# Kernel optimization log

Hardware: AMD Instinct MI355X
Metric: run time of the kernel (lower is better)

## Reference

```python
import jax, jax.numpy as jnp
import numpy as np

EPS = 1e-5
T = 5          # Newton-Schulz iterations
G = 64         # num_groups
FACTOR = 1.0   # reparameterization scale


def setup_inputs() -> dict:
    key = jax.random.key(0)
    k1, k2, k3, k4 = jax.random.split(key, 4)
    B, C, H, W = 32, 256, 64, 64
    x = jax.random.normal(k1, (B, C, H, W), dtype=jnp.float32)
    idx = jax.random.permutation(k2, C)                      # random channel shuffle
    eps1 = jax.random.normal(k3, (B, G, G), dtype=jnp.float32)  # randn_like(wm_inv)
    eps2 = jax.random.normal(k4, (B, G, 1), dtype=jnp.float32)  # randn_like(mean)
    return {"x": x, "idx": idx, "eps1": eps1, "eps2": eps2}


def _sqrtvar(t):
    # torch .var(dim=0) is unbiased (ddof=1); repeat over batch == broadcast
    return jnp.sqrt(jnp.var(t, axis=0, keepdims=True, ddof=1) + EPS)


def reference(x, idx, eps1, eps2):
    B, C, H, W = x.shape
    # reverse permutation: reverse_idx[idx[i]] = i
    reverse_idx = jnp.zeros_like(idx).at[idx].set(jnp.arange(C, dtype=idx.dtype))

    xs = x[:, idx].reshape(B, G, -1)          # [B, G, m], m = (C//G)*H*W
    m = xs.shape[-1]
    mean = xs.mean(-1, keepdims=True)         # [B, G, 1]
    xm = xs - mean

    sigma = jnp.einsum('bgm,bhm->bgh', xm, xm) / m   # [B, G, G]
    I = jnp.eye(G, dtype=x.dtype)
    trace_inv = 1.0 / jnp.trace(sigma, axis1=1, axis2=2)[:, None, None]
    sigma_N = sigma * trace_inv

    # Newton-Schulz inverse square root: P <- 1.5 P - 0.5 P^3 sigma_N
    P = jnp.broadcast_to(I, sigma.shape)
    for _ in range(T):
        P = 1.5 * P - 0.5 * ((P @ P @ P) @ sigma_N)
    wm = P * jnp.sqrt(trace_inv)

    # faithful to original b_inv: solve(I, wm) == wm (original code quirk)
    wm_inv = jnp.linalg.solve(jnp.broadcast_to(I, wm.shape), wm)

    # stochastic reparameterization of gamma (symmetrized via triu) and beta
    wir = wm_inv + (eps1 * FACTOR) * _sqrtvar(wm_inv)
    gamma = jnp.triu(wir) + jnp.swapaxes(jnp.triu(wir, k=1), 1, 2)
    beta = mean + (eps2 * FACTOR) * _sqrtvar(mean)

    y = gamma @ (wm @ xm) + beta              # [B, G, m]
    out = y.reshape(B, C, H, W)[:, reverse_idx]
    return out
```

## Files before the change

### kernel.cpp

```cpp
#include <hip/hip_runtime.h>

typedef __attribute__((ext_vector_type(8))) short short8;
typedef __attribute__((ext_vector_type(4))) short short4v;
typedef __attribute__((ext_vector_type(4))) float f32x4;

#define MFMA16 __builtin_amdgcn_mfma_f32_16x16x32_bf16

__device__ __forceinline__ short bf16t(float f) {
  return (short)(__float_as_uint(f) >> 16);
}
__device__ __forceinline__ float bf16f(short h) {
  return __uint_as_float(((unsigned)(unsigned short)h) << 16);
}

__device__ __forceinline__ void lds_barrier() {
  asm volatile("s_waitcnt lgkmcnt(0)" ::: "memory");
  __builtin_amdgcn_s_barrier();
  asm volatile("" ::: "memory");
}

__device__ __forceinline__ void mm64(const float* X, const float* Y, float* D,
                                     int tid) {
  const int R = (tid >> 4) << 2;
  const int Cc = (tid & 15) << 2;
  float acc[4][4];
#pragma unroll
  for (int i = 0; i < 4; i++)
#pragma unroll
    for (int j = 0; j < 4; j++) acc[i][j] = 0.f;
#pragma unroll 4
  for (int kk = 0; kk < 64; kk++) {
    f32x4 a = *(const f32x4*)&X[(kk << 6) + R];
    f32x4 bb = *(const f32x4*)&Y[(kk << 6) + Cc];
#pragma unroll
    for (int i = 0; i < 4; i++)
#pragma unroll
      for (int j = 0; j < 4; j++) acc[i][j] = fmaf(a[i], bb[j], acc[i][j]);
  }
#pragma unroll
  for (int i = 0; i < 4; i++) {
    f32x4 r = {acc[i][0], acc[i][1], acc[i][2], acc[i][3]};
    *(f32x4*)&D[((R + i) << 6) + Cc] = r;
  }
  __syncthreads();
}

__global__ __launch_bounds__(256, 4) void k_stats(const float* __restrict__ x,
                                                  const int* __restrict__ idx,
                                                  float* __restrict__ sigw,
                                                  float* __restrict__ rsum) {
  __shared__ __align__(16) short XT[2][2 * 64 * 72];
  __shared__ int chan[64];
  const int tid = threadIdx.x;
  const int w = tid >> 6, lane = tid & 63;
  const int q = lane >> 4, n15 = lane & 15;
  const int u = tid >> 4;
  const int quad = tid & 15;
  const int blk = blockIdx.x;
  const int b = blk >> 5, k = (blk >> 3) & 3, pc = blk & 7;

  if (tid < 64) chan[tid] = idx[(tid << 2) + k];
  __syncthreads();

  const float* xb = x + ((size_t)b << 20);
  const int pcbase = pc << 9;

  f32x4 acc[4];
#pragma unroll
  for (int t = 0; t < 4; t++) acc[t] = (f32x4){0.f, 0.f, 0.f, 0.f};
  float rsp[4] = {0.f, 0.f, 0.f, 0.f};

  f32x4 vv[4];
#pragma unroll
  for (int i = 0; i < 4; i++)
    vv[i] = *(const f32x4*)&xb[((size_t)chan[(i << 4) + u] << 12) + pcbase +
                               (quad << 2)];

  for (int c = 0; c < 8; c++) {
    short* XH = &XT[c & 1][0];
    short* XL = XH + 64 * 72;
#pragma unroll
    for (int i = 0; i < 4; i++) {
      const int ch = (i << 4) + u;
      rsp[i] += vv[i][0] + vv[i][1] + vv[i][2] + vv[i][3];
      short4v hv, lv;
#pragma unroll
      for (int j = 0; j < 4; j++) {
        hv[j] = bf16t(vv[i][j]);
        lv[j] = bf16t(vv[i][j] - bf16f(hv[j]));
      }
      *(short4v*)&XH[ch * 72 + (quad << 2)] = hv;
      *(short4v*)&XL[ch * 72 + (quad << 2)] = lv;
    }
    if (c < 7) {
      const int p0 = pcbase + ((c + 1) << 6);
#pragma unroll
      for (int i = 0; i < 4; i++)
        vv[i] = *(const f32x4*)&xb[((size_t)chan[(i << 4) + u] << 12) + p0 +
                                   (quad << 2)];
    }
    lds_barrier();
#pragma unroll
    for (int s = 0; s < 2; s++) {
      const int ko = (s << 5) + (q << 3);
      const short8 ah = *(const short8*)&XH[((w << 4) + n15) * 72 + ko];
      const short8 al = *(const short8*)&XL[((w << 4) + n15) * 72 + ko];
#pragma unroll
      for (int hb = 0; hb < 4; hb++) {
        const short8 bh = *(const short8*)&XH[((hb << 4) + n15) * 72 + ko];
        const short8 bl = *(const short8*)&XL[((hb << 4) + n15) * 72 + ko];
        acc[hb] = MFMA16(ah, bh, acc[hb], 0, 0, 0);
        acc[hb] = MFMA16(ah, bl, acc[hb], 0, 0, 0);
        acc[hb] = MFMA16(al, bh, acc[hb], 0, 0, 0);
      }
    }
  }
#pragma unroll
  for (int i = 0; i < 4; i++) {
    float r = rsp[i];
    r += __shfl_xor(r, 1);
    r += __shfl_xor(r, 2);
    r += __shfl_xor(r, 4);
    r += __shfl_xor(r, 8);
    if (quad == 0) atomicAdd(&rsum[(b << 6) + (i << 4) + u], r);
  }
  float* sb = sigw + ((size_t)b << 12);
#pragma unroll
  for (int hb = 0; hb < 4; hb++)
#pragma unroll
    for (int r = 0; r < 4; r++)
      atomicAdd(&sb[(((w << 4) + (q << 2) + r) << 6) + (hb << 4) + n15],
                acc[hb][r]);
}

#define NSTR 72

__global__ __launch_bounds__(256) void k_ns(const float* __restrict__ sigw,
                                            const float* __restrict__ rsum,
                                            float* __restrict__ meanw,
                                            float* __restrict__ wmw) {
  __shared__ __align__(16) short PA[2 * 64 * NSTR];
  __shared__ __align__(16) short TB[2 * 64 * NSTR];
  __shared__ __align__(16) short SB[2 * 64 * NSTR];
  __shared__ float ml[64];
  __shared__ float tr_s;
  const int tid = threadIdx.x;
  const int b = blockIdx.x;
  const int w = tid >> 6, lane = tid & 63;
  const int q = lane >> 4, n15 = lane & 15;

  float* SNf = (float*)TB;

  if (tid < 64) {
    const float mu = rsum[(b << 6) + tid] * (1.f / 16384.f);
    ml[tid] = mu;
    meanw[(b << 6) + tid] = mu;
  }
  __syncthreads();
#pragma unroll
  for (int i = 0; i < 16; i++) {
    const int e = (i << 8) + tid;
    const int g = e >> 6, h = e & 63;
    SNf[e] = sigw[(b << 12) + e] * (1.f / 16384.f) - ml[g] * ml[h];
  }
  __syncthreads();
  if (tid < 64) {
    float d = SNf[tid * 65];
#pragma unroll
    for (int off = 32; off; off >>= 1) d += __shfl_down(d, off);
    if (tid == 0) tr_s = 1.f / d;
  }
  __syncthreads();
  const float trinv = tr_s;

#pragma unroll
  for (int i = 0; i < 16; i++) {
    const int e = (i << 8) + tid;
    const int g = e >> 6, h = e & 63;
    const float sv = SNf[e] * trinv;
    const short sh = bf16t(sv);
    SB[g * NSTR + h] = sh;
    SB[64 * NSTR + g * NSTR + h] = bf16t(sv - bf16f(sh));
    const float pv = ((g == h) ? 1.5f : 0.f) - 0.5f * sv;
    const short ph = bf16t(pv);
    PA[g * NSTR + h] = ph;
    PA[64 * NSTR + g * NSTR + h] = bf16t(pv - bf16f(ph));
  }
  float pr[4][4];
#pragma unroll
  for (int ct = 0; ct < 4; ct++)
#pragma unroll
    for (int r = 0; r < 4; r++) {
      const int row = (w << 4) + (q << 2) + r, col = (ct << 4) + n15;
      pr[ct][r] =
          ((row == col) ? 1.5f : 0.f) - 0.5f * SNf[(row << 6) + col] * trinv;
    }
  __syncthreads();

  for (int it = 0; it < 4; it++) {
    f32x4 aP2[4], aPS[4];
#pragma unroll
    for (int t = 0; t < 4; t++) {
      aP2[t] = (f32x4){0.f, 0.f, 0.f, 0.f};
      aPS[t] = (f32x4){0.f, 0.f, 0.f, 0.f};
    }
#pragma unroll
    for (int s = 0; s < 2; s++) {
      const int ko = (s << 5) + (q << 3);
      const short8 ah = *(const short8*)&PA[((w << 4) + n15) * NSTR + ko];
      const short8 al =
          *(const short8*)&PA[64 * NSTR + ((w << 4) + n15) * NSTR + ko];
#pragma unroll
      for (int ct = 0; ct < 4; ct++) {
        const short8 bh = *(const short8*)&PA[((ct << 4) + n15) * NSTR + ko];
        const short8 bl =
            *(const short8*)&PA[64 * NSTR + ((ct << 4) + n15) * NSTR + ko];
        aP2[ct] = MFMA16(ah, bh, aP2[ct], 0, 0, 0);
        aP2[ct] = MFMA16(ah, bl, aP2[ct], 0, 0, 0);
        aP2[ct] = MFMA16(al, bh, aP2[ct], 0, 0, 0);
        const short8 ch = *(const short8*)&SB[((ct << 4) + n15) * NSTR + ko];
        const short8 cl =
            *(const short8*)&SB[64 * NSTR + ((ct << 4) + n15) * NSTR + ko];
        aPS[ct] = MFMA16(ah, ch, aPS[ct], 0, 0, 0);
        aPS[ct] = MFMA16(ah, cl, aPS[ct], 0, 0, 0);
        aPS[ct] = MFMA16(al, ch, aPS[ct], 0, 0, 0);
      }
    }
    __syncthreads();
#pragma unroll
    for (int ct = 0; ct < 4; ct++)
#pragma unroll
      for (int r = 0; r < 4; r++) {
        const int row = (w << 4) + (q << 2) + r, col = (ct << 4) + n15;
        const float v1 = aP2[ct][r];
        const short h1 = bf16t(v1);
        PA[row * NSTR + col] = h1;
        PA[64 * NSTR + row * NSTR + col] = bf16t(v1 - bf16f(h1));
        const float v2 = aPS[ct][r];
        const short h2 = bf16t(v2);
        TB[row * NSTR + col] = h2;
        TB[64 * NSTR + row * NSTR + col] = bf16t(v2 - bf16f(h2));
      }
    __syncthreads();
    f32x4 aT3[4];
#pragma unroll
    for (int t = 0; t < 4; t++) aT3[t] = (f32x4){0.f, 0.f, 0.f, 0.f};
#pragma unroll
    for (int s = 0; s < 2; s++) {
      const int ko = (s << 5) + (q << 3);
      const short8 ah = *(const short8*)&PA[((w << 4) + n15) * NSTR + ko];
      const short8 al =
          *(const short8*)&PA[64 * NSTR + ((w << 4) + n15) * NSTR + ko];
#pragma unroll
      for (int ct = 0; ct < 4; ct++) {
        const short8 bh = *(const short8*)&TB[((ct << 4) + n15) * NSTR + ko];
        const short8 bl =
            *(const short8*)&TB[64 * NSTR + ((ct << 4) + n15) * NSTR + ko];
        aT3[ct] = MFMA16(ah, bh, aT3[ct], 0, 0, 0);
        aT3[ct] = MFMA16(ah, bl, aT3[ct], 0, 0, 0);
        aT3[ct] = MFMA16(al, bh, aT3[ct], 0, 0, 0);
      }
    }
    __syncthreads();
    const bool last = (it == 3);
    const float sc = sqrtf(trinv);
#pragma unroll
    for (int ct = 0; ct < 4; ct++)
#pragma unroll
      for (int r = 0; r < 4; r++) {
        const int row = (w << 4) + (q << 2) + r, col = (ct << 4) + n15;
        const float pn = 1.5f * pr[ct][r] - 0.5f * aT3[ct][r];
        pr[ct][r] = pn;
        if (last) {
          wmw[(b << 12) + (row << 6) + col] = pn * sc;
        } else {
          const short h1 = bf16t(pn);
          PA[row * NSTR + col] = h1;
          PA[64 * NSTR + row * NSTR + col] = bf16t(pn - bf16f(h1));
        }
      }
    if (!last) __syncthreads();
  }
}

__global__ __launch_bounds__(256) void k_gA(
    const float* __restrict__ wmw, const float* __restrict__ meanw,
    const float* __restrict__ eps1, const float* __restrict__ eps2,
    short* __restrict__ Ahl, float* __restrict__ ofsw) {
  __shared__ __align__(16) float Wl[4096];
  __shared__ __align__(16) float Gm[4096];
  __shared__ __align__(16) float Al[4096];
  __shared__ float ml[64];
  __shared__ float svml[64];
  const int tid = threadIdx.x;
  const int b = blockIdx.x;
  float* Sv = Al;

#pragma unroll
  for (int i = 0; i < 16; i++) {
    const int e = (i << 8) + tid;
    float vv[32];
    float s = 0.f;
#pragma unroll
    for (int p = 0; p < 32; p++) {
      vv[p] = wmw[(p << 12) + e];
      s += vv[p];
    }
    const float mu = s * (1.f / 32.f);
    float s2 = 0.f;
#pragma unroll
    for (int p = 0; p < 32; p++) {
      const float d = vv[p] - mu;
      s2 = fmaf(d, d, s2);
    }
    Sv[e] = sqrtf(s2 * (1.f / 31.f) + 1e-5f);
  }
  if (tid < 64) {
    ml[tid] = meanw[(b << 6) + tid];
    float vv[32];
    float s = 0.f;
#pragma unroll
    for (int p = 0; p < 32; p++) {
      vv[p] = meanw[(p << 6) + tid];
      s += vv[p];
    }
    const float mu = s * (1.f / 32.f);
    float s2 = 0.f;
#pragma unroll
    for (int p = 0; p < 32; p++) {
      const float d = vv[p] - mu;
      s2 = fmaf(d, d, s2);
    }
    svml[tid] = sqrtf(s2 * (1.f / 31.f) + 1e-5f);
  }
#pragma unroll
  for (int i = 0; i < 16; i++) {
    const int e = (i << 8) + tid;
    Wl[e] = wmw[(b << 12) + e];
  }
  __syncthreads();
#pragma unroll
  for (int i = 0; i < 16; i++) {
    const int e = (i << 8) + tid;
    const int g = e >> 6, h = e & 63;
    const int eu = (h >= g) ? e : ((h << 6) + g);
    Gm[e] = Wl[eu] + eps1[(b << 12) + eu] * Sv[eu];
  }
  __syncthreads();
  mm64(Gm, Wl, Al, tid);
  short* Ab = Ahl + ((size_t)b << 13);
#pragma unroll
  for (int i = 0; i < 16; i++) {
    const int e = (i << 8) + tid;
    const float a = Al[e];
    const short h2 = bf16t(a);
    Ab[e] = h2;
    Ab[4096 + e] = bf16t(a - bf16f(h2));
  }
  if (tid < 64) {
    float dot = 0.f;
    for (int h = 0; h < 64; h++) dot = fmaf(Al[(tid << 6) + h], ml[h], dot);
    ofsw[(b << 6) + tid] = ml[tid] + eps2[(b << 6) + tid] * svml[tid] - dot;
  }
}

__global__ __launch_bounds__(256, 4) void k_apply(const float* __restrict__ x,
                                                  const int* __restrict__ idx,
                                                  const short* __restrict__ Ahl,
                                                  const float* __restrict__ ofsw,
                                                  float* __restrict__ out) {
  __shared__ __align__(16) short XT[2][2 * 64 * 72];
  __shared__ int chan[64];
  const int tid = threadIdx.x;
  const int w = tid >> 6, lane = tid & 63;
  const int q = lane >> 4, n15 = lane & 15;
  const int blk = blockIdx.x;
  const int b = blk >> 5, k = (blk >> 3) & 3, pc = blk & 7;

  if (tid < 64) chan[tid] = idx[(tid << 2) + k];

  const short* Ab = Ahl + ((size_t)b << 13);
  short8 ah[2], al[2];
#pragma unroll
  for (int s = 0; s < 2; s++) {
    const int o = (((w << 4) + n15) << 6) + (s << 5) + (q << 3);
    ah[s] = *(const short8*)&Ab[o];
    al[s] = *(const short8*)&Ab[4096 + o];
  }
  const float of = ofsw[(b << 6) + (w << 4) + n15];
  __syncthreads();

  const float* xb = x + ((size_t)b << 20);
  float* outb = out + ((size_t)b << 20);
  const int pcbase = pc << 9;

  float v[16];
#pragma unroll
  for (int j = 0; j < 16; j++)
    v[j] = xb[((size_t)chan[(w << 4) + j] << 12) + pcbase + lane];

  for (int c = 0; c < 8; c++) {
    short* XH = &XT[c & 1][0];
    short* XL = XH + 64 * 72;
#pragma unroll
    for (int jj = 0; jj < 4; jj++) {
      short4v hv, lv;
#pragma unroll
      for (int j = 0; j < 4; j++) {
        const float f = v[(jj << 2) + j];
        hv[j] = bf16t(f);
        lv[j] = bf16t(f - bf16f(hv[j]));
      }
      *(short4v*)&XH[lane * 72 + (w << 4) + (jj << 2)] = hv;
      *(short4v*)&XL[lane * 72 + (w << 4) + (jj << 2)] = lv;
    }
    if (c < 7) {
      const int p0n = pcbase + ((c + 1) << 6);
#pragma unroll
      for (int j = 0; j < 16; j++)
        v[j] = xb[((size_t)chan[(w << 4) + j] << 12) + p0n + lane];
    }
    lds_barrier();

    const int p0 = pcbase + (c << 6);
    f32x4 acc[4];
#pragma unroll
    for (int nb = 0; nb < 4; nb++) acc[nb] = (f32x4){of, of, of, of};
#pragma unroll
    for (int s = 0; s < 2; s++) {
#pragma unroll
      for (int nb = 0; nb < 4; nb++) {
        const int ro = ((nb << 4) + n15) * 72 + (s << 5) + (q << 3);
        const short8 xh = *(const short8*)&XH[ro];
        const short8 xl = *(const short8*)&XL[ro];
        acc[nb] = MFMA16(xh, ah[s], acc[nb], 0, 0, 0);
        acc[nb] = MFMA16(xl, ah[s], acc[nb], 0, 0, 0);
        acc[nb] = MFMA16(xh, al[s], acc[nb], 0, 0, 0);
      }
    }
#pragma unroll
    for (int nb = 0; nb < 4; nb++) {
      *(f32x4*)&outb[((size_t)chan[(w << 4) + n15] << 12) + p0 + (nb << 4) +
                     (q << 2)] = acc[nb];
    }
  }
}

extern "C" void kernel_launch(void* const* d_in, const int* in_sizes, int n_in,
                              void* d_out, int out_size, void* d_ws,
                              size_t ws_size, hipStream_t stream) {
  const float* x = (const float*)d_in[0];
  const int* idx = (const int*)d_in[1];
  const float* eps1 = (const float*)d_in[2];
  const float* eps2 = (const float*)d_in[3];
  float* out = (float*)d_out;
  float* ws = (float*)d_ws;

  float* sigw = ws;
  float* rsum = ws + 131072;
  float* meanw = ws + 133120;
  float* wmw = ws + 135168;
  float* ofsw = ws + 270400;
  short* Ahl = (short*)(ws + 272448);

  hipMemsetAsync(ws, 0, (131072 + 2048) * sizeof(float), stream);
  k_stats<<<1024, 256, 0, stream>>>(x, idx, sigw, rsum);
  k_ns<<<32, 256, 0, stream>>>(sigw, rsum, meanw, wmw);
  k_gA<<<32, 256, 0, stream>>>(wmw, meanw, eps1, eps2, Ahl, ofsw);
  k_apply<<<1024, 256, 0, stream>>>(x, idx, Ahl, ofsw, out);
}
```

Before: 299.5 us.

## Vectorize x loads and pack hi/lo bf16 pairs into one LDS tile

```diff
diff --git a/kernel.cpp b/kernel.cpp
--- a/kernel.cpp
+++ b/kernel.cpp
@@ -3,6 +3,7 @@
 typedef __attribute__((ext_vector_type(8))) short short8;
 typedef __attribute__((ext_vector_type(4))) short short4v;
 typedef __attribute__((ext_vector_type(4))) float f32x4;
+typedef __attribute__((ext_vector_type(4))) unsigned uint4v;
 
 #define MFMA16 __builtin_amdgcn_mfma_f32_16x16x32_bf16
 
@@ -364,16 +365,20 @@
   }
 }
 
+#define XSTR 76
+
 __global__ __launch_bounds__(256, 4) void k_apply(const float* __restrict__ x,
                                                   const int* __restrict__ idx,
                                                   const short* __restrict__ Ahl,
                                                   const float* __restrict__ ofsw,
                                                   float* __restrict__ out) {
-  __shared__ __align__(16) short XT[2][2 * 64 * 72];
+  __shared__ __align__(16) unsigned XP[2][64 * XSTR];
   __shared__ int chan[64];
   const int tid = threadIdx.x;
   const int w = tid >> 6, lane = tid & 63;
   const int q = lane >> 4, n15 = lane & 15;
+  const int u = tid >> 4;
+  const int quad = tid & 15;
   const int blk = blockIdx.x;
   const int b = blk >> 5, k = (blk >> 3) & 3, pc = blk & 7;
 
@@ -394,35 +399,37 @@
   float* outb = out + ((size_t)b << 20);
   const int pcbase = pc << 9;
 
-  float v[16];
-#pragma unroll
-  for (int j = 0; j < 16; j++)
-    v[j] = xb[((size_t)chan[(w << 4) + j] << 12) + pcbase + lane];
+  const float* rp[4];
+#pragma unroll
+  for (int i = 0; i < 4; i++)
+    rp[i] = xb + ((size_t)chan[(i << 4) + u] << 12) + pcbase + (quad << 2);
+  float* op = outb + ((size_t)chan[(w << 4) + n15] << 12) + pcbase;
+
+  f32x4 vv[4];
+#pragma unroll
+  for (int i = 0; i < 4; i++) vv[i] = *(const f32x4*)rp[i];
 
   for (int c = 0; c < 8; c++) {
-    short* XH = &XT[c & 1][0];
-    short* XL = XH + 64 * 72;
-#pragma unroll
-    for (int jj = 0; jj < 4; jj++) {
-      short4v hv, lv;
+    unsigned* XB = &XP[c & 1][0];
+#pragma unroll
+    for (int i = 0; i < 4; i++) {
+      const int ch = (i << 4) + u;
 #pragma unroll
       for (int j = 0; j < 4; j++) {
-        const float f = v[(jj << 2) + j];
-        hv[j] = bf16t(f);
-        lv[j] = bf16t(f - bf16f(hv[j]));
-      }
-      *(short4v*)&XH[lane * 72 + (w << 4) + (jj << 2)] = hv;
-      *(short4v*)&XL[lane * 72 + (w << 4) + (jj << 2)] = lv;
+        const float f = vv[i][j];
+        const short hv = bf16t(f);
+        const short lv = bf16t(f - bf16f(hv));
+        XB[((quad << 2) + j) * XSTR + ch] =
+            (((unsigned)(unsigned short)hv) << 16) | (unsigned short)lv;
+      }
     }
     if (c < 7) {
-      const int p0n = pcbase + ((c + 1) << 6);
-#pragma unroll
-      for (int j = 0; j < 16; j++)
-        v[j] = xb[((size_t)chan[(w << 4) + j] << 12) + p0n + lane];
+#pragma unroll
+      for (int i = 0; i < 4; i++)
+        vv[i] = *(const f32x4*)(rp[i] + ((c + 1) << 6));
     }
     lds_barrier();
 
-    const int p0 = pcbase + (c << 6);
     f32x4 acc[4];
 #pragma unroll
     for (int nb = 0; nb < 4; nb++) acc[nb] = (f32x4){of, of, of, of};
@@ -430,18 +437,30 @@
     for (int s = 0; s < 2; s++) {
 #pragma unroll
       for (int nb = 0; nb < 4; nb++) {
-        const int ro = ((nb << 4) + n15) * 72 + (s << 5) + (q << 3);
-        const short8 xh = *(const short8*)&XH[ro];
-        const short8 xl = *(const short8*)&XL[ro];
-        acc[nb] = MFMA16(xh, ah[s], acc[nb], 0, 0, 0);
-        acc[nb] = MFMA16(xl, ah[s], acc[nb], 0, 0, 0);
-        acc[nb] = MFMA16(xh, al[s], acc[nb], 0, 0, 0);
+        const unsigned* base =
+            &XB[((nb << 4) + n15) * XSTR + (s << 5) + (q << 3)];
+        const uint4v P0 = *(const uint4v*)base;
+        const uint4v P1 = *(const uint4v*)(base + 4);
+        union {
+          unsigned u4[4];
+          short8 s8;
+        } H, L;
+        H.u4[0] = __builtin_amdgcn_perm(P0[1], P0[0], 0x07060302u);
+        H.u4[1] = __builtin_amdgcn_perm(P0[3], P0[2], 0x07060302u);
+        H.u4[2] = __builtin_amdgcn_perm(P1[1], P1[0], 0x07060302u);
+        H.u4[3] = __builtin_amdgcn_perm(P1[3], P1[2], 0x07060302u);
+        L.u4[0] = __builtin_amdgcn_perm(P0[1], P0[0], 0x05040100u);
+        L.u4[1] = __builtin_amdgcn_perm(P0[3], P0[2], 0x05040100u);
+        L.u4[2] = __builtin_amdgcn_perm(P1[1], P1[0], 0x05040100u);
+        L.u4[3] = __builtin_amdgcn_perm(P1[3], P1[2], 0x05040100u);
+        acc[nb] = MFMA16(H.s8, ah[s], acc[nb], 0, 0, 0);
+        acc[nb] = MFMA16(L.s8, ah[s], acc[nb], 0, 0, 0);
+        acc[nb] = MFMA16(H.s8, al[s], acc[nb], 0, 0, 0);
       }
     }
 #pragma unroll
     for (int nb = 0; nb < 4; nb++) {
-      *(f32x4*)&outb[((size_t)chan[(w << 4) + n15] << 12) + p0 + (nb << 4) +
-                     (q << 2)] = acc[nb];
+      *(f32x4*)(op + (c << 6) + (nb << 4) + (q << 2)) = acc[nb];
     }
   }
 }
```

Measured after the change: 301.7 us. Within noise of the previous version (+0.7%).
